# Kernel optimization log

Measured on AMD Instinct MI355X. Metric: run time of the kernel, lower is better.

## Reference

```python
import jax, jax.numpy as jnp
import numpy as np
from numpy.lib.stride_tricks import sliding_window_view

# Static configuration matching init_kwargs
F_, H_, W_ = 2, 32, 32          # video_shape
K = 5                            # kernel_size (odd)
HEADS, DIM_HEAD = 8, 64
N = F_ * H_ * W_                 # number of video tokens (2048)
PAD = K // 2
INNER = HEADS * DIM_HEAD         # 512


def _neighbors():
    # Flattened token index at each (f,h,w); pad with sentinel N (out of bounds -> zeros / masked)
    idx = np.arange(N, dtype=np.int32).reshape(F_, H_, W_)
    padded = np.full((F_ + 2 * PAD, H_ + 2 * PAD, W_ + 2 * PAD), N, dtype=np.int32)
    padded[PAD:PAD + F_, PAD:PAD + H_, PAD:PAD + W_] = idx
    # sliding_window_view matches unfoldNd's kernel-offset ordering (kf, kh, kw row-major)
    return sliding_window_view(padded, (K, K, K)).reshape(N, K ** 3)


NBR = jnp.asarray(_neighbors())                                   # [N, K^3]
# causal: query i attends only to neighbors with index <= i; prepend BOS column (never masked)
CAUSAL = jnp.pad(jnp.arange(N)[:, None] < NBR, ((0, 0), (1, 0)))  # [N, K^3 + 1]


def setup_inputs() -> dict:
    key = jax.random.key(0)
    k1, k2, k3 = jax.random.split(key, 3)
    return {
        "x": jax.random.normal(k1, (1, N, INNER), jnp.float32),
        "w_qkv": jax.random.normal(k2, (INNER, 3 * INNER), jnp.float32) * 0.02,
        "w_out": jax.random.normal(k3, (INNER, INNER), jnp.float32) * 0.02,
        "b_out": jnp.zeros((INNER,), jnp.float32),
    }


def reference(x, w_qkv, w_out, b_out):
    b, n, dim = x.shape            # n == N
    bh = b * HEADS
    scale = DIM_HEAD ** -0.5

    xp = jnp.pad(x, ((0, 0), (0, 1), (0, 0)))        # pad one zero token at the end: [b, n+1, dim]
    qkv = xp @ w_qkv                                  # [b, n+1, 3*inner]
    q, kk, vv = jnp.split(qkv, 3, axis=-1)

    def split_heads(t):  # 'b n (h d) -> (b h) n d'
        return t.reshape(b, n + 1, HEADS, DIM_HEAD).transpose(0, 2, 1, 3).reshape(bh, n + 1, DIM_HEAD)

    q, kk, vv = map(split_heads, (q, kk, vv))
    q = q[:, 1:] * scale                              # drop BOS query: [bh, n, d]
    k_bos, kk = kk[:, :1], kk[:, 1:]                  # BOS kv + n spatial tokens
    v_bos, vv = vv[:, :1], vv[:, 1:]

    # Append a zero row so the sentinel index N gathers zeros (== unfold's zero padding)
    zero = jnp.zeros((bh, 1, DIM_HEAD), kk.dtype)
    kw = jnp.concatenate([kk, zero], axis=1)[:, NBR]  # [bh, n, K^3, d]
    vw = jnp.concatenate([vv, zero], axis=1)[:, NBR]

    bos_k = jnp.broadcast_to(k_bos[:, None], (bh, n, 1, DIM_HEAD))
    bos_v = jnp.broadcast_to(v_bos[:, None], (bh, n, 1, DIM_HEAD))
    kw = jnp.concatenate([bos_k, kw], axis=2)         # [bh, n, K^3+1, d]
    vw = jnp.concatenate([bos_v, vw], axis=2)

    sim = jnp.einsum('bid,bijd->bij', q, kw)          # [bh, n, K^3+1]
    sim = jnp.where(CAUSAL[:n], -jnp.finfo(sim.dtype).max, sim)
    attn = jax.nn.softmax(sim, axis=-1)
    out = jnp.einsum('bij,bijd->bid', attn, vw)       # [bh, n, d]

    out = jnp.concatenate([v_bos, out], axis=1)       # BOS output = its value: [bh, n+1, d]
    out = out.reshape(b, HEADS, n + 1, DIM_HEAD).transpose(0, 2, 1, 3).reshape(b, n + 1, INNER)
    return (out @ w_out + b_out)[:, :n]
```

## Files before the change

### kernel.cpp

```cpp
#include <hip/hip_runtime.h>
#include <hip/hip_bf16.h>

#define NTOK  2048
#define INNER 512
#define KDIM  512
#define QKVP  1536

typedef __attribute__((ext_vector_type(8))) short bf16x8;
typedef __attribute__((ext_vector_type(4))) float f32x4;

__device__ __forceinline__ unsigned short f2b(float f) {
  unsigned int u = __float_as_uint(f);
  return (unsigned short)((u + 0x7FFFu + ((u >> 16) & 1u)) >> 16);
}

__device__ __forceinline__ void async_copy16(const unsigned short* g, unsigned short* l) {
  __builtin_amdgcn_global_load_lds((const __attribute__((address_space(1))) void*)g,
                                   (__attribute__((address_space(3))) void*)l, 16, 0, 0);
}

__global__ __launch_bounds__(256) void prep(const float* __restrict__ w_qkv,
                                            const float* __restrict__ w_out,
                                            const float* __restrict__ x,
                                            unsigned short* __restrict__ wqkvT,
                                            unsigned short* __restrict__ woutT,
                                            unsigned short* __restrict__ xb,
                                            int* __restrict__ glist,
                                            int* __restrict__ gcnt) {
  __shared__ float tile[32][33];
  __shared__ int list[192];
  __shared__ int cntS;
  const int tid = threadIdx.x;
  int b = blockIdx.x;

  if (b >= 1152) {
    const int i = (b - 1152) * 1024 + tid * 4;
    float4 v = *(const float4*)(x + i);
    ushort4 o;
    o.x = f2b(v.x); o.y = f2b(v.y); o.z = f2b(v.z); o.w = f2b(v.w);
    *(ushort4*)(xb + i) = o;
    return;
  }

  if (b < 1024) {
    const float* in; unsigned short* out; int K, N, bx, by;
    if (b < 768) { in = w_qkv; out = wqkvT; K = 512; N = 1536; bx = b % 48; by = b / 48; }
    else { int bb = b - 768; in = w_out; out = woutT; K = 512; N = 512; bx = bb & 15; by = bb >> 4; }
    const int k0 = by * 32, n0 = bx * 32;
    const int r = tid >> 3, c4 = (tid & 7) * 4;
    float4 v = *(const float4*)(in + (size_t)(k0 + r) * N + n0 + c4);
    tile[r][c4 + 0] = v.x; tile[r][c4 + 1] = v.y;
    tile[r][c4 + 2] = v.z; tile[r][c4 + 3] = v.w;
    __syncthreads();
    ushort4 o;
    o.x = f2b(tile[c4 + 0][r]);
    o.y = f2b(tile[c4 + 1][r]);
    o.z = f2b(tile[c4 + 2][r]);
    o.w = f2b(tile[c4 + 3][r]);
    *(ushort4*)(out + (size_t)(n0 + r) * K + k0 + c4) = o;
    return;
  }

  const int pt = b - 1024;
  const int f  = pt >> 6;
  const int hh = (pt >> 1) & 31;
  const int w0 = (pt & 1) << 4;

  if (tid < 192) list[tid] = 0x7FFFFFFF;
  if (tid == 0) { list[0] = 0; cntS = 1; }
  __syncthreads();
  if (tid >= 1 && tid <= 160) {
    int cc = tid - 1;
    int p = cc / 20, wo = cc - p * 20;
    int ff = (p < 5) ? 0 : 1;
    int h2 = hh - 2 + ((p < 5) ? p : (p - 5));
    bool ok = (p < 5) ? ((f == 1) ? (h2 >= 0 && h2 <= 31) : (p <= 2 && h2 >= 0))
                      : (f == 1 && h2 >= 0);
    if (ok) {
      bool diag = (ff == f) && (h2 == hh);
      int wlo = max(0, w0 - 2);
      int whi = min(31, diag ? (w0 + 15) : (w0 + 17));
      int w2 = wlo + wo;
      if (w2 <= whi) {
        int pos = atomicAdd(&cntS, 1);
        list[pos] = ((ff << 10) | (h2 << 5) | w2) + 1;
      }
    }
  }
  __syncthreads();
  if (tid < 192) glist[pt * 192 + tid] = list[tid];
  if (tid == 0) gcnt[pt] = cntS;
}

__global__ __launch_bounds__(256, 4) void gemm_qkv(const unsigned short* __restrict__ A,
                                                   const unsigned short* __restrict__ Bt,
                                                   unsigned short* __restrict__ C) {
  constexpr int N = 1536, K = 512;
  __shared__ __align__(16) unsigned short As[2][2][64 * 32];
  __shared__ __align__(16) unsigned short Bs[2][2][64 * 32];
  const int tid = threadIdx.x, lane = tid & 63, wave = tid >> 6;
  const int m0 = blockIdx.y * 64, n0 = blockIdx.x * 64;
  const int wm = (wave >> 1) * 32, wn = (wave & 1) * 32;
  const int li = tid * 8, r = li >> 5, c = li & 31;
  const int fr = lane & 15, fk = (lane >> 4) * 8;

  f32x4 acc[2][2] = {};

#define STG1(buf, kk)                                                              \
  do {                                                                             \
    async_copy16(A  + (size_t)(m0 + r) * K + (kk) + c,      &As[buf][0][li]);      \
    async_copy16(A  + (size_t)(m0 + r) * K + (kk) + 32 + c, &As[buf][1][li]);      \
    async_copy16(Bt + (size_t)(n0 + r) * K + (kk) + c,      &Bs[buf][0][li]);      \
    async_copy16(Bt + (size_t)(n0 + r) * K + (kk) + 32 + c, &Bs[buf][1][li]);      \
  } while (0)

  STG1(0, 0);
#pragma unroll
  for (int it = 0; it < 8; ++it) {
    const int cur = it & 1;
    if (it < 7) {
      STG1(cur ^ 1, (it + 1) * 64);
      asm volatile("s_waitcnt vmcnt(4)" ::: "memory");
    } else {
      asm volatile("s_waitcnt vmcnt(0)" ::: "memory");
    }
    __builtin_amdgcn_s_barrier();
    __builtin_amdgcn_sched_barrier(0);
    bf16x8 af[2][2], bfr[2][2];
#pragma unroll
    for (int h = 0; h < 2; ++h) {
#pragma unroll
      for (int i = 0; i < 2; ++i) af[i][h]  = *(const bf16x8*)&As[cur][h][(wm + i * 16 + fr) * 32 + fk];
#pragma unroll
      for (int j = 0; j < 2; ++j) bfr[j][h] = *(const bf16x8*)&Bs[cur][h][(wn + j * 16 + fr) * 32 + fk];
    }
#pragma unroll
    for (int i = 0; i < 2; ++i)
#pragma unroll
      for (int j = 0; j < 2; ++j) {
        acc[i][j] = __builtin_amdgcn_mfma_f32_16x16x32_bf16(af[i][0], bfr[j][0], acc[i][j], 0, 0, 0);
        acc[i][j] = __builtin_amdgcn_mfma_f32_16x16x32_bf16(af[i][1], bfr[j][1], acc[i][j], 0, 0, 0);
      }
    __builtin_amdgcn_s_barrier();
  }
#undef STG1

  const int er = (lane >> 4) * 4, ec = lane & 15;
#pragma unroll
  for (int i = 0; i < 2; ++i)
#pragma unroll
    for (int j = 0; j < 2; ++j) {
      const int col = n0 + wn + j * 16 + ec;
#pragma unroll
      for (int rr = 0; rr < 4; ++rr) {
        const int row = m0 + wm + i * 16 + er + rr;
        C[(size_t)row * N + col] = f2b(acc[i][j][rr]);
      }
    }
}

__global__ __launch_bounds__(256, 4) void gemm_out(const unsigned short* __restrict__ A,
                                                   const unsigned short* __restrict__ Bt,
                                                   const float* __restrict__ bias,
                                                   float* __restrict__ C) {
  constexpr int N = 512, K = 512;
  __shared__ __align__(16) unsigned short As[2][2][32 * 32];
  __shared__ __align__(16) unsigned short Bs[2][2][64 * 32];
  const int tid = threadIdx.x, lane = tid & 63, wave = tid >> 6;
  const int m0 = blockIdx.y * 32, n0 = blockIdx.x * 64;
  const int wm = (wave >> 1) * 16, wn = (wave & 1) * 32;
  const int li = tid * 8, r = li >> 5, c = li & 31;
  const int fr = lane & 15, fk = (lane >> 4) * 8;

  f32x4 acc[2] = {};

#define STG2(buf, kk)                                                               \
  do {                                                                              \
    if (tid < 128) {                                                                \
      async_copy16(A + (size_t)(m0 + r) * K + (kk) + c,      &As[buf][0][li]);      \
      async_copy16(A + (size_t)(m0 + r) * K + (kk) + 32 + c, &As[buf][1][li]);      \
    }                                                                               \
    async_copy16(Bt + (size_t)(n0 + r) * K + (kk) + c,      &Bs[buf][0][li]);       \
    async_copy16(Bt + (size_t)(n0 + r) * K + (kk) + 32 + c, &Bs[buf][1][li]);       \
  } while (0)

  STG2(0, 0);
#pragma unroll
  for (int it = 0; it < 8; ++it) {
    const int cur = it & 1;
    if (it < 7) {
      STG2(cur ^ 1, (it + 1) * 64);
      if (wave < 2) asm volatile("s_waitcnt vmcnt(4)" ::: "memory");
      else          asm volatile("s_waitcnt vmcnt(2)" ::: "memory");
    } else {
      asm volatile("s_waitcnt vmcnt(0)" ::: "memory");
    }
    __builtin_amdgcn_s_barrier();
    __builtin_amdgcn_sched_barrier(0);
    bf16x8 af[2], bfr[2][2];
#pragma unroll
    for (int h = 0; h < 2; ++h) {
      af[h] = *(const bf16x8*)&As[cur][h][(wm + fr) * 32 + fk];
#pragma unroll
      for (int j = 0; j < 2; ++j) bfr[j][h] = *(const bf16x8*)&Bs[cur][h][(wn + j * 16 + fr) * 32 + fk];
    }
#pragma unroll
    for (int j = 0; j < 2; ++j) {
      acc[j] = __builtin_amdgcn_mfma_f32_16x16x32_bf16(af[0], bfr[j][0], acc[j], 0, 0, 0);
      acc[j] = __builtin_amdgcn_mfma_f32_16x16x32_bf16(af[1], bfr[j][1], acc[j], 0, 0, 0);
    }
    __builtin_amdgcn_s_barrier();
  }
#undef STG2

  const int er = (lane >> 4) * 4, ec = lane & 15;
#pragma unroll
  for (int j = 0; j < 2; ++j) {
    const int col = n0 + wn + j * 16 + ec;
    const float b = bias[col];
#pragma unroll
    for (int rr = 0; rr < 4; ++rr) {
      const int row = m0 + wm + er + rr;
      C[(size_t)row * N + col] = acc[j][rr] + b;
    }
  }
}

__global__ __launch_bounds__(256, 4) void attn_mfma(const unsigned short* __restrict__ qkv,
                                                    const int* __restrict__ glist,
                                                    const int* __restrict__ gcnt,
                                                    unsigned short* __restrict__ O) {
  __shared__ __align__(16) int list[192];
  __shared__ __align__(16) unsigned short Vlds[4][16 * 72];
  __shared__ __align__(16) float mOd[3][16][72];
  __shared__ float mM[3][16], mL[3][16];
  __shared__ int cntS;

  const int tid  = threadIdx.x;
  const int head = blockIdx.y;

  if (blockIdx.x == 128) {
    if (tid < 64) O[head * 64 + tid] = qkv[1024 + head * 64 + tid];
    return;
  }
  const int pt = blockIdx.x;
  const int f  = pt >> 6;
  const int hh = (pt >> 1) & 31;
  const int w0 = (pt & 1) << 4;
  const int base_i = (f << 10) | (hh << 5) | w0;

  if (tid < 192) list[tid] = glist[pt * 192 + tid];
  if (tid == 0) cntS = gcnt[pt];
  __syncthreads();
  const int nsub = (cntS + 15) >> 4;

  const int lane = tid & 63;
  const int wave = tid >> 6;
  const int quad = lane >> 4;
  const int ec   = lane & 15;

  const int i_q = base_i + ec;
  const int tq  = min(i_q + 1, 2047);
  const unsigned short* qrow = qkv + (size_t)tq * QKVP + head * 64 + quad * 8;
  const bf16x8 qb0 = *(const bf16x8*)(qrow);
  const bf16x8 qb1 = *(const bf16x8*)(qrow + 32);

  unsigned short* vbuf = &Vlds[wave][0];

  f32x4 Od[4] = {{0,0,0,0},{0,0,0,0},{0,0,0,0},{0,0,0,0}};
  float m = -1e30f, l = 0.0f;

  for (int sub = wave; sub < nsub; sub += 4) {
    const int base = sub * 16;
    const int tok_e = list[base + ec];
    const int4 tokv = *(const int4*)&list[base + quad * 4];
    const int tk[4] = {tokv.x, tokv.y, tokv.z, tokv.w};

    const int t0 = (tok_e > 2047) ? 0 : tok_e;
    const unsigned short* kr = qkv + (size_t)t0 * QKVP + 512 + head * 64 + quad * 8;
    const unsigned short* vr = qkv + (size_t)t0 * QKVP + 1024 + head * 64 + quad * 8;
    const bf16x8 kf0 = *(const bf16x8*)(kr);
    const bf16x8 kf1 = *(const bf16x8*)(kr + 32);
    const bf16x8 vs0 = *(const bf16x8*)(vr);
    const bf16x8 vs1 = *(const bf16x8*)(vr + 32);

    f32x4 S = {0, 0, 0, 0};
    S = __builtin_amdgcn_mfma_f32_16x16x32_bf16(kf0, qb0, S, 0, 0, 0);
    S = __builtin_amdgcn_mfma_f32_16x16x32_bf16(kf1, qb1, S, 0, 0, 0);

    *(bf16x8*)&vbuf[ec * 72 + quad * 8]      = vs0;
    *(bf16x8*)&vbuf[ec * 72 + 32 + quad * 8] = vs1;

    float Sm[4];
#pragma unroll
    for (int r = 0; r < 4; ++r) {
      const int tok = tk[r];
      const int idx = tok - 1;
      const bool v = (tok == 0) ||
                     ((idx <= i_q) && ((unsigned)((idx & 31) - (w0 + ec) + 2) <= 4u));
      Sm[r] = v ? S[r] * 0.125f : -1e30f;
    }
    float mx = fmaxf(fmaxf(Sm[0], Sm[1]), fmaxf(Sm[2], Sm[3]));
    mx = fmaxf(mx, __shfl_xor(mx, 16, 64));
    mx = fmaxf(mx, __shfl_xor(mx, 32, 64));
    const float mn = fmaxf(m, mx);
    const float corr = __expf(m - mn);
    m = mn;
    const float p0 = __expf(Sm[0] - mn);
    const float p1 = __expf(Sm[1] - mn);
    const float p2 = __expf(Sm[2] - mn);
    const float p3 = __expf(Sm[3] - mn);
    float rs = (p0 + p1) + (p2 + p3);
    rs += __shfl_xor(rs, 16, 64);
    rs += __shfl_xor(rs, 32, 64);
    l = l * corr + rs;

    bf16x8 pf;
    pf[0] = (short)f2b(p0); pf[1] = (short)f2b(p1);
    pf[2] = (short)f2b(p2); pf[3] = (short)f2b(p3);
    pf[4] = 0; pf[5] = 0; pf[6] = 0; pf[7] = 0;

#pragma unroll
    for (int dt = 0; dt < 4; ++dt) {
      bf16x8 vf;
#pragma unroll
      for (int j = 0; j < 4; ++j) vf[j] = (short)vbuf[(quad * 4 + j) * 72 + dt * 16 + ec];
      vf[4] = 0; vf[5] = 0; vf[6] = 0; vf[7] = 0;
#pragma unroll
      for (int r = 0; r < 4; ++r) Od[dt][r] *= corr;
      Od[dt] = __builtin_amdgcn_mfma_f32_16x16x32_bf16(vf, pf, Od[dt], 0, 0, 0);
    }
  }

  if (wave > 0) {
#pragma unroll
    for (int dt = 0; dt < 4; ++dt)
      *(f32x4*)&mOd[wave - 1][ec][dt * 16 + quad * 4] = Od[dt];
    if (quad == 0) { mM[wave - 1][ec] = m; mL[wave - 1][ec] = l; }
  }
  __syncthreads();
  if (wave == 0 && i_q <= 2046) {
    const float m1 = mM[0][ec], m2 = mM[1][ec], m3 = mM[2][ec];
    const float mm = fmaxf(fmaxf(m, m1), fmaxf(m2, m3));
    const float c0 = __expf(m - mm);
    const float c1 = __expf(m1 - mm);
    const float c2 = __expf(m2 - mm);
    const float c3 = __expf(m3 - mm);
    const float rl = 1.0f / (l * c0 + mL[0][ec] * c1 + mL[1][ec] * c2 + mL[2][ec] * c3);
    unsigned short* ob = O + (size_t)(i_q + 1) * 512 + head * 64 + quad * 4;
#pragma unroll
    for (int dt = 0; dt < 4; ++dt) {
      const f32x4 o1 = *(const f32x4*)&mOd[0][ec][dt * 16 + quad * 4];
      const f32x4 o2 = *(const f32x4*)&mOd[1][ec][dt * 16 + quad * 4];
      const f32x4 o3 = *(const f32x4*)&mOd[2][ec][dt * 16 + quad * 4];
      ushort4 u;
      u.x = f2b((Od[dt][0] * c0 + o1[0] * c1 + o2[0] * c2 + o3[0] * c3) * rl);
      u.y = f2b((Od[dt][1] * c0 + o1[1] * c1 + o2[1] * c2 + o3[1] * c3) * rl);
      u.z = f2b((Od[dt][2] * c0 + o1[2] * c1 + o2[2] * c2 + o3[2] * c3) * rl);
      u.w = f2b((Od[dt][3] * c0 + o1[3] * c1 + o2[3] * c2 + o3[3] * c3) * rl);
      *(ushort4*)(ob + dt * 16) = u;
    }
  }
}


extern "C" void kernel_launch(void* const* d_in, const int* in_sizes, int n_in,
                              void* d_out, int out_size, void* d_ws, size_t ws_size,
                              hipStream_t stream) {
  const float* x     = (const float*)d_in[0];
  const float* w_qkv = (const float*)d_in[1];
  const float* w_out = (const float*)d_in[2];
  const float* b_out = (const float*)d_in[3];
  float* out = (float*)d_out;

  char* ws = (char*)d_ws;
  unsigned short* qkvb  = (unsigned short*)(ws);
  unsigned short* wqkvT = (unsigned short*)(ws + 6291456);
  unsigned short* woutT = (unsigned short*)(ws + 7864320);
  unsigned short* Ob    = (unsigned short*)(ws + 8388608);
  unsigned short* xb    = (unsigned short*)(ws + 10485760);
  int*            glist = (int*)(ws + 12582912);
  int*            gcnt  = (int*)(ws + 12681216);

  hipLaunchKernelGGL(prep, dim3(2176), dim3(256), 0, stream,
                     w_qkv, w_out, x, wqkvT, woutT, xb, glist, gcnt);

  hipLaunchKernelGGL(gemm_qkv, dim3(24, 32), dim3(256), 0, stream, xb, wqkvT, qkvb);

  hipLaunchKernelGGL(attn_mfma, dim3(129, 8), dim3(256), 0, stream, qkvb, glist, gcnt, Ob);

  hipLaunchKernelGGL(gemm_out, dim3(8, 64), dim3(256), 0, stream, Ob, woutT, b_out, out);
}
```

Baseline: 88.37 us.

## Process 32 neighbors per attention step and remap GEMM blocks per XCD

```diff
diff --git a/kernel.cpp b/kernel.cpp
--- a/kernel.cpp
+++ b/kernel.cpp
@@ -99,7 +99,11 @@
   __shared__ __align__(16) unsigned short As[2][2][64 * 32];
   __shared__ __align__(16) unsigned short Bs[2][2][64 * 32];
   const int tid = threadIdx.x, lane = tid & 63, wave = tid >> 6;
-  const int m0 = blockIdx.y * 64, n0 = blockIdx.x * 64;
+  const int bid = blockIdx.x;
+  const int xcd = bid & 7, idx = bid >> 3;
+  const int rm = idx & 7, rn = idx >> 3;
+  const int m0 = (((xcd >> 1) << 3) + rm) * 64;
+  const int n0 = ((xcd & 1) * 12 + rn) * 64;
   const int wm = (wave >> 1) * 32, wn = (wave & 1) * 32;
   const int li = tid * 8, r = li >> 5, c = li & 31;
   const int fr = lane & 15, fk = (lane >> 4) * 8;
@@ -167,7 +171,11 @@
   __shared__ __align__(16) unsigned short As[2][2][32 * 32];
   __shared__ __align__(16) unsigned short Bs[2][2][64 * 32];
   const int tid = threadIdx.x, lane = tid & 63, wave = tid >> 6;
-  const int m0 = blockIdx.y * 32, n0 = blockIdx.x * 64;
+  const int bid = blockIdx.x;
+  const int xcd = bid & 7, idx = bid >> 3;
+  const int rm = idx & 15, rn = idx >> 4;
+  const int m0 = (((xcd >> 1) << 4) + rm) * 32;
+  const int n0 = ((xcd & 1) * 4 + rn) * 64;
   const int wm = (wave >> 1) * 16, wn = (wave & 1) * 32;
   const int li = tid * 8, r = li >> 5, c = li & 31;
   const int fr = lane & 15, fk = (lane >> 4) * 8;
@@ -231,7 +239,7 @@
                                                     const int* __restrict__ gcnt,
                                                     unsigned short* __restrict__ O) {
   __shared__ __align__(16) int list[192];
-  __shared__ __align__(16) unsigned short Vlds[4][16 * 72];
+  __shared__ __align__(16) unsigned short Vlds[4][32 * 72];
   __shared__ __align__(16) float mOd[3][16][72];
   __shared__ float mM[3][16], mL[3][16];
   __shared__ int cntS;
@@ -252,7 +260,7 @@
   if (tid < 192) list[tid] = glist[pt * 192 + tid];
   if (tid == 0) cntS = gcnt[pt];
   __syncthreads();
-  const int nsub = (cntS + 15) >> 4;
+  const int nsub32 = (cntS + 31) >> 5;
 
   const int lane = tid & 63;
   const int wave = tid >> 6;
@@ -270,62 +278,86 @@
   f32x4 Od[4] = {{0,0,0,0},{0,0,0,0},{0,0,0,0},{0,0,0,0}};
   float m = -1e30f, l = 0.0f;
 
-  for (int sub = wave; sub < nsub; sub += 4) {
-    const int base = sub * 16;
-    const int tok_e = list[base + ec];
-    const int4 tokv = *(const int4*)&list[base + quad * 4];
-    const int tk[4] = {tokv.x, tokv.y, tokv.z, tokv.w};
-
-    const int t0 = (tok_e > 2047) ? 0 : tok_e;
-    const unsigned short* kr = qkv + (size_t)t0 * QKVP + 512 + head * 64 + quad * 8;
-    const unsigned short* vr = qkv + (size_t)t0 * QKVP + 1024 + head * 64 + quad * 8;
-    const bf16x8 kf0 = *(const bf16x8*)(kr);
-    const bf16x8 kf1 = *(const bf16x8*)(kr + 32);
-    const bf16x8 vs0 = *(const bf16x8*)(vr);
-    const bf16x8 vs1 = *(const bf16x8*)(vr + 32);
-
-    f32x4 S = {0, 0, 0, 0};
-    S = __builtin_amdgcn_mfma_f32_16x16x32_bf16(kf0, qb0, S, 0, 0, 0);
-    S = __builtin_amdgcn_mfma_f32_16x16x32_bf16(kf1, qb1, S, 0, 0, 0);
-
-    *(bf16x8*)&vbuf[ec * 72 + quad * 8]      = vs0;
-    *(bf16x8*)&vbuf[ec * 72 + 32 + quad * 8] = vs1;
-
-    float Sm[4];
+  for (int sub = wave; sub < nsub32; sub += 4) {
+    const int base = sub * 32;
+    const int tokA = list[base + ec];
+    const int tokB = list[base + 16 + ec];
+    const int4 tkvA = *(const int4*)&list[base + quad * 4];
+    const int4 tkvB = *(const int4*)&list[base + 16 + quad * 4];
+
+    const int tA = (tokA > 2047) ? 0 : tokA;
+    const int tB = (tokB > 2047) ? 0 : tokB;
+    const unsigned short* krA = qkv + (size_t)tA * QKVP + 512 + head * 64 + quad * 8;
+    const unsigned short* vrA = qkv + (size_t)tA * QKVP + 1024 + head * 64 + quad * 8;
+    const unsigned short* krB = qkv + (size_t)tB * QKVP + 512 + head * 64 + quad * 8;
+    const unsigned short* vrB = qkv + (size_t)tB * QKVP + 1024 + head * 64 + quad * 8;
+    const bf16x8 kA0 = *(const bf16x8*)(krA);
+    const bf16x8 kA1 = *(const bf16x8*)(krA + 32);
+    const bf16x8 kB0 = *(const bf16x8*)(krB);
+    const bf16x8 kB1 = *(const bf16x8*)(krB + 32);
+    const bf16x8 vA0 = *(const bf16x8*)(vrA);
+    const bf16x8 vA1 = *(const bf16x8*)(vrA + 32);
+    const bf16x8 vB0 = *(const bf16x8*)(vrB);
+    const bf16x8 vB1 = *(const bf16x8*)(vrB + 32);
+
+    f32x4 SA = {0, 0, 0, 0}, SB = {0, 0, 0, 0};
+    SA = __builtin_amdgcn_mfma_f32_16x16x32_bf16(kA0, qb0, SA, 0, 0, 0);
+    SA = __builtin_amdgcn_mfma_f32_16x16x32_bf16(kA1, qb1, SA, 0, 0, 0);
+    SB = __builtin_amdgcn_mfma_f32_16x16x32_bf16(kB0, qb0, SB, 0, 0, 0);
+    SB = __builtin_amdgcn_mfma_f32_16x16x32_bf16(kB1, qb1, SB, 0, 0, 0);
+
+    *(bf16x8*)&vbuf[ec * 72 + quad * 8]             = vA0;
+    *(bf16x8*)&vbuf[ec * 72 + 32 + quad * 8]        = vA1;
+    *(bf16x8*)&vbuf[(16 + ec) * 72 + quad * 8]      = vB0;
+    *(bf16x8*)&vbuf[(16 + ec) * 72 + 32 + quad * 8] = vB1;
+
+    const int tka[4] = {tkvA.x, tkvA.y, tkvA.z, tkvA.w};
+    const int tkb[4] = {tkvB.x, tkvB.y, tkvB.z, tkvB.w};
+    float Sm[8];
 #pragma unroll
     for (int r = 0; r < 4; ++r) {
-      const int tok = tk[r];
-      const int idx = tok - 1;
-      const bool v = (tok == 0) ||
-                     ((idx <= i_q) && ((unsigned)((idx & 31) - (w0 + ec) + 2) <= 4u));
-      Sm[r] = v ? S[r] * 0.125f : -1e30f;
-    }
-    float mx = fmaxf(fmaxf(Sm[0], Sm[1]), fmaxf(Sm[2], Sm[3]));
+      {
+        const int tok = tka[r];
+        const int idx = tok - 1;
+        const bool v = (tok == 0) ||
+                       ((idx <= i_q) && ((unsigned)((idx & 31) - (w0 + ec) + 2) <= 4u));
+        Sm[r] = v ? SA[r] * 0.125f : -1e30f;
+      }
+      {
+        const int tok = tkb[r];
+        const int idx = tok - 1;
+        const bool v = (tok == 0) ||
+                       ((idx <= i_q) && ((unsigned)((idx & 31) - (w0 + ec) + 2) <= 4u));
+        Sm[4 + r] = v ? SB[r] * 0.125f : -1e30f;
+      }
+    }
+    float mx = fmaxf(fmaxf(fmaxf(Sm[0], Sm[1]), fmaxf(Sm[2], Sm[3])),
+                     fmaxf(fmaxf(Sm[4], Sm[5]), fmaxf(Sm[6], Sm[7])));
     mx = fmaxf(mx, __shfl_xor(mx, 16, 64));
     mx = fmaxf(mx, __shfl_xor(mx, 32, 64));
     const float mn = fmaxf(m, mx);
     const float corr = __expf(m - mn);
     m = mn;
-    const float p0 = __expf(Sm[0] - mn);
-    const float p1 = __expf(Sm[1] - mn);
-    const float p2 = __expf(Sm[2] - mn);
-    const float p3 = __expf(Sm[3] - mn);
-    float rs = (p0 + p1) + (p2 + p3);
+    float p[8];
+#pragma unroll
+    for (int i = 0; i < 8; ++i) p[i] = __expf(Sm[i] - mn);
+    float rs = ((p[0] + p[1]) + (p[2] + p[3])) + ((p[4] + p[5]) + (p[6] + p[7]));
     rs += __shfl_xor(rs, 16, 64);
     rs += __shfl_xor(rs, 32, 64);
     l = l * corr + rs;
 
     bf16x8 pf;
-    pf[0] = (short)f2b(p0); pf[1] = (short)f2b(p1);
-    pf[2] = (short)f2b(p2); pf[3] = (short)f2b(p3);
-    pf[4] = 0; pf[5] = 0; pf[6] = 0; pf[7] = 0;
+#pragma unroll
+    for (int i = 0; i < 8; ++i) pf[i] = (short)f2b(p[i]);
 
 #pragma unroll
     for (int dt = 0; dt < 4; ++dt) {
       bf16x8 vf;
 #pragma unroll
-      for (int j = 0; j < 4; ++j) vf[j] = (short)vbuf[(quad * 4 + j) * 72 + dt * 16 + ec];
-      vf[4] = 0; vf[5] = 0; vf[6] = 0; vf[7] = 0;
+      for (int j = 0; j < 4; ++j) {
+        vf[j]     = (short)vbuf[(quad * 4 + j) * 72 + dt * 16 + ec];
+        vf[4 + j] = (short)vbuf[(16 + quad * 4 + j) * 72 + dt * 16 + ec];
+      }
 #pragma unroll
       for (int r = 0; r < 4; ++r) Od[dt][r] *= corr;
       Od[dt] = __builtin_amdgcn_mfma_f32_16x16x32_bf16(vf, pf, Od[dt], 0, 0, 0);
@@ -385,9 +417,9 @@
   hipLaunchKernelGGL(prep, dim3(2176), dim3(256), 0, stream,
                      w_qkv, w_out, x, wqkvT, woutT, xb, glist, gcnt);
 
-  hipLaunchKernelGGL(gemm_qkv, dim3(24, 32), dim3(256), 0, stream, xb, wqkvT, qkvb);
+  hipLaunchKernelGGL(gemm_qkv, dim3(768), dim3(256), 0, stream, xb, wqkvT, qkvb);
 
   hipLaunchKernelGGL(attn_mfma, dim3(129, 8), dim3(256), 0, stream, qkvb, glist, gcnt, Ob);
 
-  hipLaunchKernelGGL(gemm_out, dim3(8, 64), dim3(256), 0, stream, Ob, woutT, b_out, out);
-}
+  hipLaunchKernelGGL(gemm_out, dim3(512), dim3(256), 0, stream, Ob, woutT, b_out, out);
+}
```

Measured after the change: 90.16 us. +2.0%, slower.
